# Optimization experiments

Hardware: AMD Instinct MI355X
Metric: run time of the kernel (lower is better)

Reference implementation:

```python
import jax, jax.numpy as jnp
import numpy as np

N = 8192        # nodes
E = 49152       # edges (~avg degree 6, triangular mesh)
H = 6           # GATv2 heads
C = 512         # hidden_size (per-head out channels)
F_IN = 2 + C    # GATv2 in_channels = coord(2) + hidden(512)
ALL_FEAT = 37   # deform_in_c-2 + 16 + 16
NUM_LOOP = 3
LRELU_SLOPE = 0.2


def setup_inputs() -> dict:
    key = jax.random.key(0)
    ks = jax.random.split(key, 10)
    x = jax.random.uniform(ks[0], (N, 7), dtype=jnp.float32)
    local_feat = jax.random.normal(ks[1], (N, 16), dtype=jnp.float32)
    conv_feat = jax.random.normal(ks[2], (N, 16), dtype=jnp.float32)
    edge_index = jax.random.randint(ks[3], (2, E), 0, N, dtype=jnp.int64)
    bd_mask = jnp.zeros((N,), jnp.int32)  # poly_mesh=False path
    W_lin = jax.random.normal(ks[4], (ALL_FEAT, C), dtype=jnp.float32) / np.float32(np.sqrt(ALL_FEAT))
    b_lin = jnp.zeros((C,), jnp.float32)
    Wl = jax.random.normal(ks[5], (F_IN, H * C), dtype=jnp.float32) / np.float32(np.sqrt(F_IN))
    Wr = jax.random.normal(ks[6], (F_IN, H * C), dtype=jnp.float32) / np.float32(np.sqrt(F_IN))
    att = jax.random.normal(ks[7], (H, C), dtype=jnp.float32) / np.float32(np.sqrt(C))
    gat_bias = jnp.zeros((C,), jnp.float32)
    W_coord = jax.random.normal(ks[8], (C, 2), dtype=jnp.float32) / np.float32(np.sqrt(C))
    b_coord = jnp.zeros((2,), jnp.float32)
    return dict(x=x, local_feat=local_feat, conv_feat=conv_feat,
                W_lin=W_lin, b_lin=b_lin, Wl=Wl, Wr=Wr, att=att,
                gat_bias=gat_bias, W_coord=W_coord, b_coord=b_coord,
                edge_index=edge_index, bd_mask=bd_mask)


def _gatv2(feat, src, dst, Wl, Wr, att, bias):
    # PyG GATv2Conv: lin_l on source, lin_r on target, additive attention
    n = feat.shape[0]
    xl = (feat @ Wl).reshape(n, H, C)            # source-side transform
    xr = (feat @ Wr).reshape(n, H, C)            # target-side transform
    e = xl[src] + xr[dst]                        # [E', H, C]
    e = jax.nn.leaky_relu(e, LRELU_SLOPE)
    logits = jnp.einsum('ehc,hc->eh', e, att)    # [E', H]
    m = jax.ops.segment_max(logits, dst, num_segments=n)
    m = jnp.where(jnp.isfinite(m), m, 0.0)
    a = jnp.exp(logits - m[dst])
    denom = jax.ops.segment_sum(a, dst, num_segments=n) + 1e-16
    alpha = a / denom[dst]                       # segment softmax over incoming edges
    msg = xl[src] * alpha[:, :, None]            # [E', H, C]
    out = jax.ops.segment_sum(msg, dst, num_segments=n)  # [N, H, C]
    return out.mean(axis=1) + bias               # concat=False -> mean over heads


def reference(x, local_feat, conv_feat, W_lin, b_lin, Wl, Wr, att, gat_bias,
              W_coord, b_coord, edge_index, bd_mask):
    coord = x[:, :2]
    hidden_in = jnp.concatenate([x[:, 2:], local_feat, conv_feat], axis=1)
    hidden = jax.nn.selu(hidden_in @ W_lin + b_lin)
    # GATv2Conv adds self-loops by default
    loops = jnp.arange(N, dtype=edge_index.dtype)
    src = jnp.concatenate([edge_index[0], loops])
    dst = jnp.concatenate([edge_index[1], loops])
    for _ in range(NUM_LOOP):
        up = coord[:, 0] == 1.0
        down = coord[:, 0] == 0.0
        left = coord[:, 1] == 0.0
        right = coord[:, 1] == 1.0
        feat = jnp.concatenate([coord, hidden], axis=1)   # [N, 514]
        hidden = jax.nn.selu(_gatv2(feat, src, dst, Wl, Wr, att, gat_bias))
        out = hidden @ W_coord + b_coord                  # [N, 2]
        ox = jnp.where(down, 0.0, jnp.where(up, 1.0, out[:, 0]))
        oy = jnp.where(right, 1.0, jnp.where(left, 0.0, out[:, 1]))
        coord = jnp.stack([ox, oy], axis=1)
    return coord
```

## Files before the change

### kernel.cpp

```cpp
#include <hip/hip_runtime.h>
#include <hip/hip_bf16.h>
#include <math.h>

#define N_NODES   8192
#define NUM_E     49152
#define NUM_EDGES (NUM_E + N_NODES)
#define H_HEADS   6
#define C_DIM     512
#define HC        (H_HEADS * C_DIM)
#define XLR       (2 * HC)
#define N_FEAT    37
#define LRELU_SLOPE 0.2f
#define SELU_LAMBDA 1.0507009873554805f
#define SELU_ALPHA  1.6732632423543772f

typedef __bf16 bf16_t;
typedef bf16_t bf16x8 __attribute__((ext_vector_type(8)));
typedef float  f32x4  __attribute__((ext_vector_type(4)));
typedef float  f32x2  __attribute__((ext_vector_type(2)));

__device__ __forceinline__ int edge_src(const int* ei, int e) {
    return e < NUM_E ? ei[e] : (e - NUM_E);
}
__device__ __forceinline__ int edge_dst(const int* ei, int e) {
    return e < NUM_E ? ei[NUM_E + e] : (e - NUM_E);
}
__device__ __forceinline__ float selu_f(float v) {
    return v > 0.f ? SELU_LAMBDA * v : SELU_LAMBDA * SELU_ALPHA * (__expf(v) - 1.f);
}
__device__ __forceinline__ void gload_lds16(const void* g, void* l) {
    __builtin_amdgcn_global_load_lds((const __attribute__((address_space(1))) void*)g,
                                     (__attribute__((address_space(3))) void*)l, 16, 0, 0);
}

__global__ __launch_bounds__(512) void k_hidden0(
    const float* __restrict__ x, const float* __restrict__ lf,
    const float* __restrict__ cf, const float* __restrict__ W,
    const float* __restrict__ b, bf16_t* __restrict__ hidden,
    float* __restrict__ coord)
{
    int n = blockIdx.x;
    int c = threadIdx.x;
    __shared__ float f[N_FEAT];
    if (c < 5)            f[c] = x[n*7 + 2 + c];
    else if (c < 21)      f[c] = lf[n*16 + (c-5)];
    else if (c < N_FEAT)  f[c] = cf[n*16 + (c-21)];
    if (c < 2) coord[n*2 + c] = x[n*7 + c];
    __syncthreads();
    float acc = b[c];
    #pragma unroll
    for (int k = 0; k < N_FEAT; ++k) acc = fmaf(f[k], W[k*C_DIM + c], acc);
    hidden[n*C_DIM + c] = (bf16_t)selu_f(acc);
}

__global__ __launch_bounds__(256) void k_wt_transpose(const float* __restrict__ W,
                                                      bf16_t* __restrict__ WT)
{
    __shared__ float tile[32][33];
    int k0 = blockIdx.y * 32;
    int n0 = blockIdx.x * 32;
    int tx = threadIdx.x & 31, ty = threadIdx.x >> 5;
    #pragma unroll
    for (int i = 0; i < 4; ++i)
        tile[ty + i*8][tx] = W[(size_t)(k0 + 2 + ty + i*8) * HC + n0 + tx];
    __syncthreads();
    #pragma unroll
    for (int i = 0; i < 4; ++i)
        WT[(size_t)(n0 + ty + i*8) * C_DIM + k0 + tx] = (bf16_t)tile[tx][ty + i*8];
}

__global__ void k_hist(const int* __restrict__ ei, int* __restrict__ counts) {
    int e = blockIdx.x * blockDim.x + threadIdx.x;
    if (e >= NUM_EDGES) return;
    atomicAdd(&counts[edge_dst(ei, e)], 1);
}

__global__ __launch_bounds__(256) void k_scan(const int* __restrict__ counts,
                                              int* __restrict__ row_ptr,
                                              int* __restrict__ cursor) {
    __shared__ int part[256];
    __shared__ int off[257];
    int t = threadIdx.x;
    int base = t * 32;
    int local[32];
    int s = 0;
    #pragma unroll
    for (int i = 0; i < 32; ++i) { local[i] = s; s += counts[base + i]; }
    part[t] = s;
    __syncthreads();
    if (t == 0) {
        off[0] = 0;
        for (int i = 0; i < 256; ++i) off[i+1] = off[i] + part[i];
    }
    __syncthreads();
    int o = off[t];
    #pragma unroll
    for (int i = 0; i < 32; ++i) {
        int v = o + local[i];
        row_ptr[base + i] = v;
        cursor[base + i]  = v;
    }
    if (t == 255) row_ptr[N_NODES] = off[256];
}

__global__ void k_scatter(const int* __restrict__ ei, int* __restrict__ cursor,
                          int* __restrict__ csr_eid) {
    int e = blockIdx.x * blockDim.x + threadIdx.x;
    if (e >= NUM_EDGES) return;
    int pos = atomicAdd(&cursor[edge_dst(ei, e)], 1);
    csr_eid[pos] = e;
}

#define GM 128
#define GN 128
#define GK 32
__global__ __launch_bounds__(256) void k_gemm_bf16(
    const bf16_t* __restrict__ A,
    const bf16_t* __restrict__ BT,
    const float*  __restrict__ Wl,
    const float*  __restrict__ Wr,
    const float*  __restrict__ coord,
    bf16_t* __restrict__ out)
{
    __shared__ bf16_t As[GM][GK];
    __shared__ bf16_t Bs[GN][GK];
    int tid  = threadIdx.x;
    int wave = tid >> 6;
    int lane = tid & 63;
    int rowBase = blockIdx.y * GM;
    int colBase = blockIdx.x * GN;
    int wr = (wave >> 1) * 64;
    int wc = (wave & 1) * 64;

    f32x4 acc[4][4] = {};

    int gsw = (((lane & 3) ^ ((lane >> 3) & 3))) * 8;
    const bf16_t* Ag = A  + (size_t)(rowBase + wave*32 + (lane >> 2)) * C_DIM + gsw;
    const bf16_t* Bg = BT + (size_t)(colBase + wave*32 + (lane >> 2)) * C_DIM + gsw;
    int m16 = lane & 15;
    int q8s = (((lane >> 4) ^ ((lane >> 1) & 3))) * 8;

    for (int k0 = 0; k0 < C_DIM; k0 += GK) {
        gload_lds16(Ag + k0,            &As[wave*32     ][0]);
        gload_lds16(Ag + k0 + 16*C_DIM, &As[wave*32 + 16][0]);
        gload_lds16(Bg + k0,            &Bs[wave*32     ][0]);
        gload_lds16(Bg + k0 + 16*C_DIM, &Bs[wave*32 + 16][0]);
        __syncthreads();
        bf16x8 af[4], bfr[4];
        #pragma unroll
        for (int i = 0; i < 4; ++i) af[i]  = *(const bf16x8*)&As[wr + i*16 + m16][q8s];
        #pragma unroll
        for (int j = 0; j < 4; ++j) bfr[j] = *(const bf16x8*)&Bs[wc + j*16 + m16][q8s];
        #pragma unroll
        for (int i = 0; i < 4; ++i)
            #pragma unroll
            for (int j = 0; j < 4; ++j)
                acc[i][j] = __builtin_amdgcn_mfma_f32_16x16x32_bf16(af[i], bfr[j], acc[i][j], 0, 0, 0);
        __syncthreads();
    }

    const float* Wtop = (colBase < HC) ? Wl : Wr;
    int coff = (colBase < HC) ? 0 : HC;

    int ccol  = lane & 15;
    int crow4 = (lane >> 4) * 4;
    #pragma unroll
    for (int i = 0; i < 4; ++i) {
        #pragma unroll
        for (int r = 0; r < 4; ++r) {
            int row = rowBase + wr + i*16 + crow4 + r;
            float c0 = coord[row*2 + 0], c1 = coord[row*2 + 1];
            size_t rb = (size_t)row * XLR;
            #pragma unroll
            for (int j = 0; j < 4; ++j) {
                int col = colBase + wc + j*16 + ccol;
                int wcol = col - coff;
                out[rb + col] = (bf16_t)(acc[i][j][r] + c0 * Wtop[wcol] + c1 * Wtop[HC + wcol]);
            }
        }
    }
}

#define MAX_DEG 128
__global__ __launch_bounds__(384) void k_attn_agg(
    const bf16_t* __restrict__ xlr,
    const int* __restrict__ row_ptr, const int* __restrict__ csr_eid,
    const int* __restrict__ ei, const float* __restrict__ att,
    const float* __restrict__ gat_bias, const float* __restrict__ W_coord,
    const float* __restrict__ b_coord, const float* __restrict__ coord_in,
    bf16_t* __restrict__ hidden, float* __restrict__ coord_out)
{
    int n = blockIdx.x;
    int tid = threadIdx.x;
    int h = tid >> 6, lane = tid & 63;
    __shared__ int   s_src[MAX_DEG];
    __shared__ float s_acc[HC];
    __shared__ float s_red[12];

    int beg = row_ptr[n];
    int deg = min(row_ptr[n + 1] - beg, MAX_DEG);
    for (int j = tid; j < deg; j += 384) s_src[j] = edge_src(ei, csr_eid[beg + j]);
    __syncthreads();

    size_t off = (size_t)h * C_DIM + lane * 8;
    bf16x8 xrv = *(const bf16x8*)(xlr + (size_t)n * XLR + HC + off);
    f32x2 xr2[4], at2[4], ac2[4] = {};
    #pragma unroll
    for (int i = 0; i < 4; ++i) {
        xr2[i] = f32x2{(float)xrv[2*i], (float)xrv[2*i+1]};
        at2[i] = f32x2{att[off + 2*i], att[off + 2*i + 1]};
    }

    float l = 0.f;
    int j = 0;
    for (; j + 2 <= deg; j += 2) {
        bf16x8 xa = *(const bf16x8*)(xlr + (size_t)s_src[j]     * XLR + off);
        bf16x8 xb = *(const bf16x8*)(xlr + (size_t)s_src[j + 1] * XLR + off);
        f32x2 xla[4], xlb[4];
        #pragma unroll
        for (int i = 0; i < 4; ++i) {
            xla[i] = f32x2{(float)xa[2*i], (float)xa[2*i+1]};
            xlb[i] = f32x2{(float)xb[2*i], (float)xb[2*i+1]};
        }
        f32x2 sa = {0.f, 0.f}, sb = {0.f, 0.f};
        #pragma unroll
        for (int i = 0; i < 4; ++i) {
            f32x2 va = xla[i] + xr2[i];
            f32x2 vb = xlb[i] + xr2[i];
            sa += __builtin_elementwise_max(va, va * LRELU_SLOPE) * at2[i];
            sb += __builtin_elementwise_max(vb, vb * LRELU_SLOPE) * at2[i];
        }
        float suma = sa.x + sa.y, sumb = sb.x + sb.y;
        #pragma unroll
        for (int o = 1; o < 64; o <<= 1) {
            suma += __shfl_xor(suma, o);
            sumb += __shfl_xor(sumb, o);
        }
        float aa = __expf(suma), ab = __expf(sumb);
        l += aa + ab;
        #pragma unroll
        for (int i = 0; i < 4; ++i) ac2[i] += aa * xla[i] + ab * xlb[i];
    }
    if (j < deg) {
        bf16x8 xa = *(const bf16x8*)(xlr + (size_t)s_src[j] * XLR + off);
        f32x2 xla[4];
        #pragma unroll
        for (int i = 0; i < 4; ++i) xla[i] = f32x2{(float)xa[2*i], (float)xa[2*i+1]};
        f32x2 sa = {0.f, 0.f};
        #pragma unroll
        for (int i = 0; i < 4; ++i) {
            f32x2 va = xla[i] + xr2[i];
            sa += __builtin_elementwise_max(va, va * LRELU_SLOPE) * at2[i];
        }
        float suma = sa.x + sa.y;
        #pragma unroll
        for (int o = 1; o < 64; o <<= 1) suma += __shfl_xor(suma, o);
        float aa = __expf(suma);
        l += aa;
        #pragma unroll
        for (int i = 0; i < 4; ++i) ac2[i] += aa * xla[i];
    }

    float invl = 1.f / (l + 1e-16f) * (1.f / 6.f);
    #pragma unroll
    for (int i = 0; i < 4; ++i) {
        s_acc[off + 2*i]     = ac2[i].x * invl;
        s_acc[off + 2*i + 1] = ac2[i].y * invl;
    }
    __syncthreads();

    float p0 = 0.f, p1 = 0.f;
    for (int c = tid; c < C_DIM; c += 384) {
        float s = 0.f;
        #pragma unroll
        for (int hh = 0; hh < H_HEADS; ++hh) s += s_acc[hh * C_DIM + c];
        float hv = selu_f(s + gat_bias[c]);
        hidden[n * C_DIM + c] = (bf16_t)hv;
        p0 = fmaf(hv, W_coord[c * 2 + 0], p0);
        p1 = fmaf(hv, W_coord[c * 2 + 1], p1);
    }
    #pragma unroll
    for (int o = 32; o > 0; o >>= 1) { p0 += __shfl_down(p0, o); p1 += __shfl_down(p1, o); }
    if (lane == 0) { s_red[h * 2] = p0; s_red[h * 2 + 1] = p1; }
    __syncthreads();
    if (tid == 0) {
        float o0 = b_coord[0], o1 = b_coord[1];
        #pragma unroll
        for (int w = 0; w < H_HEADS; ++w) { o0 += s_red[w * 2]; o1 += s_red[w * 2 + 1]; }
        float cx = coord_in[n * 2 + 0], cy = coord_in[n * 2 + 1];
        float ox = (cx == 0.0f) ? 0.f : ((cx == 1.0f) ? 1.f : o0);
        float oy = (cy == 1.0f) ? 1.f : ((cy == 0.0f) ? 0.f : o1);
        coord_out[n * 2 + 0] = ox;
        coord_out[n * 2 + 1] = oy;
    }
}

extern "C" void kernel_launch(void* const* d_in, const int* in_sizes, int n_in,
                              void* d_out, int out_size, void* d_ws, size_t ws_size,
                              hipStream_t stream)
{
    const float* x       = (const float*)d_in[0];
    const float* lf      = (const float*)d_in[1];
    const float* cf      = (const float*)d_in[2];
    const float* W_lin   = (const float*)d_in[3];
    const float* b_lin   = (const float*)d_in[4];
    const float* Wl      = (const float*)d_in[5];
    const float* Wr      = (const float*)d_in[6];
    const float* att     = (const float*)d_in[7];
    const float* gbias   = (const float*)d_in[8];
    const float* W_coord = (const float*)d_in[9];
    const float* b_coord = (const float*)d_in[10];
    const int*   ei      = (const int*)d_in[11];

    char* w = (char*)d_ws;
    auto alloc = [&](size_t bytes) { char* p = w; w += (bytes + 255) & ~255ull; return p; };
    bf16_t*   hidden  = (bf16_t*)alloc((size_t)N_NODES * C_DIM * 2);
    bf16_t*   WT      = (bf16_t*)alloc((size_t)XLR * C_DIM * 2);
    bf16_t*   xlr     = (bf16_t*)alloc((size_t)N_NODES * XLR * 2);
    int*      counts  = (int*)alloc((size_t)N_NODES * 4);
    int*      row_ptr = (int*)alloc((size_t)(N_NODES + 1) * 4);
    int*      cursor  = (int*)alloc((size_t)N_NODES * 4);
    int*      csr_eid = (int*)alloc((size_t)NUM_EDGES * 4);
    float*    cA      = (float*)alloc((size_t)N_NODES * 2 * 4);
    float*    cB      = (float*)alloc((size_t)N_NODES * 2 * 4);

    hipMemsetAsync(counts, 0, (size_t)N_NODES * 4, stream);
    k_hidden0<<<N_NODES, 512, 0, stream>>>(x, lf, cf, W_lin, b_lin, hidden, cA);
    {
        dim3 tg(HC / 32, C_DIM / 32);
        k_wt_transpose<<<tg, 256, 0, stream>>>(Wl, WT);
        k_wt_transpose<<<tg, 256, 0, stream>>>(Wr, WT + (size_t)HC * C_DIM);
    }
    k_hist<<<(NUM_EDGES + 255) / 256, 256, 0, stream>>>(ei, counts);
    k_scan<<<1, 256, 0, stream>>>(counts, row_ptr, cursor);
    k_scatter<<<(NUM_EDGES + 255) / 256, 256, 0, stream>>>(ei, cursor, csr_eid);

    float* cin = cA;
    for (int it = 0; it < 3; ++it) {
        float* cout = (it == 2) ? (float*)d_out : ((it == 0) ? cB : cA);
        dim3 g(XLR / GN, N_NODES / GM);
        k_gemm_bf16<<<g, 256, 0, stream>>>(hidden, WT, Wl, Wr, cin, xlr);
        k_attn_agg<<<N_NODES, 384, 0, stream>>>(xlr, row_ptr, csr_eid, ei, att,
                                                gbias, W_coord, b_coord, cin, hidden, cout);
        cin = cout;
    }
}
```

Before: 590.7 us.

## Triple-buffer LDS tiles in bf16 GEMM with async prefetch two stages ahead

Replaces the single-buffered LDS loop in the projection GEMM with a three-slot ring buffer. Global-to-LDS loads run two K-steps ahead, and one barrier per iteration is gated by a vmcnt wait instead of two __syncthreads. The goal is to hide global load latency behind MFMA work and drop one barrier per step. It triples LDS use to 48KB per block, which may lower occupancy, and depends on hand-written waitcnt counts being correct.

```diff
diff --git a/kernel.cpp b/kernel.cpp
--- a/kernel.cpp
+++ b/kernel.cpp
@@ -114,6 +114,7 @@
 #define GM 128
 #define GN 128
 #define GK 32
+#define KITERS (C_DIM / GK)
 __global__ __launch_bounds__(256) void k_gemm_bf16(
     const bf16_t* __restrict__ A,
     const bf16_t* __restrict__ BT,
@@ -122,8 +123,8 @@
     const float*  __restrict__ coord,
     bf16_t* __restrict__ out)
 {
-    __shared__ bf16_t As[GM][GK];
-    __shared__ bf16_t Bs[GN][GK];
+    __shared__ bf16_t As[3][GM][GK];
+    __shared__ bf16_t Bs[3][GM][GK];
     int tid  = threadIdx.x;
     int wave = tid >> 6;
     int lane = tid & 63;
@@ -140,23 +141,36 @@
     int m16 = lane & 15;
     int q8s = (((lane >> 4) ^ ((lane >> 1) & 3))) * 8;
 
-    for (int k0 = 0; k0 < C_DIM; k0 += GK) {
-        gload_lds16(Ag + k0,            &As[wave*32     ][0]);
-        gload_lds16(Ag + k0 + 16*C_DIM, &As[wave*32 + 16][0]);
-        gload_lds16(Bg + k0,            &Bs[wave*32     ][0]);
-        gload_lds16(Bg + k0 + 16*C_DIM, &Bs[wave*32 + 16][0]);
-        __syncthreads();
+    auto stage = [&](int k0, int b) {
+        gload_lds16(Ag + k0,            &As[b][wave*32     ][0]);
+        gload_lds16(Ag + k0 + 16*C_DIM, &As[b][wave*32 + 16][0]);
+        gload_lds16(Bg + k0,            &Bs[b][wave*32     ][0]);
+        gload_lds16(Bg + k0 + 16*C_DIM, &Bs[b][wave*32 + 16][0]);
+    };
+
+    stage(0, 0);
+    stage(GK, 1);
+
+    int b0 = 0, b1 = 1, b2 = 2;
+    #pragma unroll 1
+    for (int t = 0; t < KITERS; ++t) {
+        if (t == KITERS - 1) asm volatile("s_waitcnt vmcnt(0)" ::: "memory");
+        else                 asm volatile("s_waitcnt vmcnt(4)" ::: "memory");
+        asm volatile("s_barrier" ::: "memory");
+        if (t + 2 < KITERS) stage((t + 2) * GK, b2);
+
         bf16x8 af[4], bfr[4];
         #pragma unroll
-        for (int i = 0; i < 4; ++i) af[i]  = *(const bf16x8*)&As[wr + i*16 + m16][q8s];
-        #pragma unroll
-        for (int j = 0; j < 4; ++j) bfr[j] = *(const bf16x8*)&Bs[wc + j*16 + m16][q8s];
+        for (int i = 0; i < 4; ++i) af[i]  = *(const bf16x8*)&As[b0][wr + i*16 + m16][q8s];
+        #pragma unroll
+        for (int j = 0; j < 4; ++j) bfr[j] = *(const bf16x8*)&Bs[b0][wc + j*16 + m16][q8s];
         #pragma unroll
         for (int i = 0; i < 4; ++i)
             #pragma unroll
             for (int j = 0; j < 4; ++j)
                 acc[i][j] = __builtin_amdgcn_mfma_f32_16x16x32_bf16(af[i], bfr[j], acc[i][j], 0, 0, 0);
-        __syncthreads();
+
+        int tmp = b0; b0 = b1; b1 = b2; b2 = tmp;
     }
 
     const float* Wtop = (colBase < HC) ? Wl : Wr;
```

Result: no change. 593.2 us (+0.4%).
